# Performance work log

Hardware: AMD Instinct MI355X
Metric: run time of the kernel (lower is better)

## Reference

```python
import jax, jax.numpy as jnp
import numpy as np

P = 22536   # priors
B = 32      # batch
M = 16      # objects per image (fixed for jit)
C = 81      # classes incl. background
THRESHOLD = 0.5
ALPHA_REG = 1.0   # config.reg_weights
FL_ALPHA = 0.25
FL_GAMMA = 2.0
EPS = 1e-7


def cxcy_to_xy(c):
    return jnp.concatenate([c[..., :2] - c[..., 2:] / 2, c[..., :2] + c[..., 2:] / 2], -1)


def gcxgcy_to_cxcy(g, p):
    return jnp.concatenate([g[..., :2] * p[..., 2:] / 10 + p[..., :2],
                            jnp.exp(g[..., 2:] / 5) * p[..., 2:]], -1)


def iou_xy(a, b):
    # a: (M,4) xyxy, b: (P,4) xyxy -> (M,P)
    lt = jnp.maximum(a[:, None, :2], b[None, :, :2])
    rb = jnp.minimum(a[:, None, 2:], b[None, :, 2:])
    inter = jnp.prod(jnp.clip(rb - lt, 0.0), -1)
    area_a = jnp.prod(a[:, 2:] - a[:, :2], -1)
    area_b = jnp.prod(b[:, 2:] - b[:, :2], -1)
    return inter / (area_a[:, None] + area_b[None, :] - inter)


def diou_loss(p, g):
    # elementwise DIoU loss, p/g: (..., 4) xyxy -> (...)
    lt = jnp.maximum(p[..., :2], g[..., :2])
    rb = jnp.minimum(p[..., 2:], g[..., 2:])
    inter = jnp.prod(jnp.clip(rb - lt, 0.0), -1)
    ap = jnp.prod(p[..., 2:] - p[..., :2], -1)
    ag = jnp.prod(g[..., 2:] - g[..., :2], -1)
    iou = inter / (ap + ag - inter + EPS)
    cp = (p[..., :2] + p[..., 2:]) / 2
    cg = (g[..., :2] + g[..., 2:]) / 2
    d2 = jnp.sum((cp - cg) ** 2, -1)
    elt = jnp.minimum(p[..., :2], g[..., :2])
    erb = jnp.maximum(p[..., 2:], g[..., 2:])
    c2 = jnp.sum((erb - elt) ** 2, -1) + EPS
    return 1.0 - iou + d2 / c2


def match_image(boxes_i, labels_i, priors_xy):
    # boxes_i: (M,4), labels_i: (M,), priors_xy: (P,4)
    overlap = iou_xy(boxes_i, priors_xy)                 # (M,P)
    ofp = overlap.max(0)                                  # overlap_for_each_prior (P,)
    obj = jnp.argmax(overlap, 0)                          # object_for_each_prior (P,)
    pfo = jnp.argmax(overlap, 1)                          # prior_for_each_object (M,)
    obj = obj.at[pfo].set(jnp.arange(M))
    ofp = ofp.at[pfo].set(1.0)
    lab = labels_i[obj]                                   # (P,)
    lab_neg = jnp.where(ofp < THRESHOLD - 0.1, -1, lab)
    lab = jnp.where(ofp < THRESHOLD, 0, lab)
    true_locs = boxes_i[obj]                              # (P,4)
    return lab, lab_neg, true_locs


def setup_inputs() -> dict:
    key = jax.random.key(0)
    k1, k2, k3, k4, k5, k6, k7 = jax.random.split(key, 7)
    pcxy = jax.random.uniform(k1, (P, 2), minval=0.05, maxval=0.95)
    pwh = jax.random.uniform(k2, (P, 2), minval=0.02, maxval=0.3)
    priors_cxcy = jnp.concatenate([pcxy, pwh], -1)
    ctr = jax.random.uniform(k3, (B, M, 2), minval=0.2, maxval=0.8)
    wh = jax.random.uniform(k4, (B, M, 2), minval=0.05, maxval=0.3)
    boxes = jnp.concatenate([ctr - wh / 2, ctr + wh / 2], -1)
    labels = jax.random.randint(k5, (B, M), 1, C).astype(jnp.int32)
    predicted_locs = jax.random.normal(k6, (B, P, 4), dtype=jnp.float32)
    predicted_scores = jax.random.normal(k7, (B, P, C), dtype=jnp.float32)
    return {"predicted_locs": predicted_locs, "predicted_scores": predicted_scores,
            "boxes": boxes, "labels": labels, "priors_cxcy": priors_cxcy}


def reference(predicted_locs, predicted_scores, boxes, labels, priors_cxcy):
    priors_xy = cxcy_to_xy(priors_cxcy)
    lab, lab_neg, true_locs = jax.vmap(match_image, in_axes=(0, 0, None))(boxes, labels, priors_xy)
    decoded = cxcy_to_xy(gcxgcy_to_cxcy(predicted_locs, priors_cxcy))   # (B,P,4)
    pos = lab > 0
    neg = lab_neg == -1
    # DIoU localization loss, mean over positive priors
    loc = diou_loss(decoded, true_locs)                                 # (B,P)
    npos = jnp.maximum(pos.sum(), 1)
    loc_loss = jnp.sum(loc * pos) / npos
    # focal classification loss over union of positive and hard-negative priors
    logp = jax.nn.log_softmax(predicted_scores, -1)                     # (B,P,C)
    lp_t = jnp.take_along_axis(logp, lab[..., None], -1)[..., 0]        # (B,P)
    pt = jnp.exp(lp_t)
    fl = FL_ALPHA * (1.0 - pt) ** FL_GAMMA * (-lp_t)
    m = pos | neg
    conf_loss = jnp.sum(fl * m) / jnp.maximum(m.sum(), 1)
    return conf_loss + ALPHA_REG * loc_loss
```

## Files before the change

kernel.cpp:

```cpp
#include <hip/hip_runtime.h>
#include <math.h>

#define PN 22536
#define BN 32
#define MN 16
#define CN 81
#define NMB ((PN + 255) / 256)
#define NCB 2048

#if __has_builtin(__builtin_amdgcn_exp2f)
#define EXP2(x) __builtin_amdgcn_exp2f(x)
#else
#define EXP2(x) exp2f(x)
#endif
#if __has_builtin(__builtin_amdgcn_logf)
#define LOG2(x) __builtin_amdgcn_logf(x)
#else
#define LOG2(x) log2f(x)
#endif

__global__ __launch_bounds__(256)
void pfo_kernel(const float* __restrict__ boxes,
                const float* __restrict__ priors,
                unsigned long long* __restrict__ pfo_key)
{
    const int b = blockIdx.y;
    const int p = blockIdx.x * 256 + threadIdx.x;

    __shared__ float4 sbox[MN];
    __shared__ float  sarea[MN];
    __shared__ unsigned long long skey[MN];
    if (threadIdx.x < MN) {
        float4 bx = reinterpret_cast<const float4*>(boxes)[b * MN + threadIdx.x];
        sbox[threadIdx.x]  = bx;
        sarea[threadIdx.x] = (bx.z - bx.x) * (bx.w - bx.y);
        skey[threadIdx.x]  = 0ull;
    }
    __syncthreads();

    float x0 = 0.f, y0 = 0.f, x1 = 0.f, y1 = 0.f, ab = 0.f;
    const bool valid = (p < PN);
    if (valid) {
        float4 pc = reinterpret_cast<const float4*>(priors)[p];
        float hw = pc.z / 2.0f, hh = pc.w / 2.0f;
        x0 = pc.x - hw; y0 = pc.y - hh;
        x1 = pc.x + hw; y1 = pc.y + hh;
        ab = (x1 - x0) * (y1 - y0);
    }

    const int lane = threadIdx.x & 63;
    #pragma unroll
    for (int m = 0; m < MN; ++m) {
        unsigned long long key = 0ull;
        if (valid) {
            float4 bx = sbox[m];
            float lx = fmaxf(bx.x, x0), ly = fmaxf(bx.y, y0);
            float rx = fminf(bx.z, x1), ry = fminf(bx.w, y1);
            float inter = fmaxf(rx - lx, 0.0f) * fmaxf(ry - ly, 0.0f);
            float iou = inter / (sarea[m] + ab - inter);
            key = ((unsigned long long)__float_as_uint(iou) << 32) |
                  (unsigned long long)(~(unsigned int)p);
        }
        #pragma unroll
        for (int off = 32; off >= 1; off >>= 1) {
            unsigned long long o = __shfl_down(key, (unsigned)off, 64);
            if (o > key) key = o;
        }
        if (lane == 0) atomicMax(&skey[m], key);
    }
    __syncthreads();
    if (threadIdx.x < MN)
        atomicMax(&pfo_key[b * MN + threadIdx.x], skey[threadIdx.x]);
}

__global__ __launch_bounds__(256)
void match_kernel(const float* __restrict__ boxes,
                  const int*   __restrict__ labels,
                  const float* __restrict__ priors,
                  const float* __restrict__ plocs,
                  const unsigned long long* __restrict__ pfo_key,
                  unsigned char* __restrict__ labbyte,
                  float4* __restrict__ mpart)
{
    const int b = blockIdx.y;
    const int p = blockIdx.x * 256 + threadIdx.x;

    __shared__ float4 sbox[MN];
    __shared__ float  sarea[MN];
    __shared__ int    slab[MN];
    __shared__ int    spfo[MN];
    __shared__ float  sred[4][3];

    if (threadIdx.x < MN) {
        float4 bx = reinterpret_cast<const float4*>(boxes)[b * MN + threadIdx.x];
        sbox[threadIdx.x]  = bx;
        sarea[threadIdx.x] = (bx.z - bx.x) * (bx.w - bx.y);
        slab[threadIdx.x]  = labels[b * MN + threadIdx.x];
        spfo[threadIdx.x]  = (int)(~(unsigned int)(pfo_key[b * MN + threadIdx.x] &
                                                   0xFFFFFFFFull));
    }
    __syncthreads();

    float loc = 0.f, mc = 0.f, psc = 0.f;
    if (p < PN) {
        float4 pc = reinterpret_cast<const float4*>(priors)[p];
        float hw = pc.z / 2.0f, hh = pc.w / 2.0f;
        float qx0 = pc.x - hw, qy0 = pc.y - hh;
        float qx1 = pc.x + hw, qy1 = pc.y + hh;
        float ab  = (qx1 - qx0) * (qy1 - qy0);

        float best = -1.0f;
        int bestm = 0;
        #pragma unroll
        for (int m = 0; m < MN; ++m) {
            float4 bx = sbox[m];
            float lx = fmaxf(bx.x, qx0), ly = fmaxf(bx.y, qy0);
            float rx = fminf(bx.z, qx1), ry = fminf(bx.w, qy1);
            float inter = fmaxf(rx - lx, 0.0f) * fmaxf(ry - ly, 0.0f);
            float iou = inter / (sarea[m] + ab - inter);
            if (iou > best) { best = iou; bestm = m; }
        }
        #pragma unroll
        for (int m = 0; m < MN; ++m)
            if (spfo[m] == p) { bestm = m; best = 1.0f; }

        bool pos = best >= 0.5f;
        bool neg = best < 0.4f;
        labbyte[(size_t)b * PN + p] =
            pos ? (unsigned char)slab[bestm] : (neg ? (unsigned char)0
                                                    : (unsigned char)255);
        if (pos || neg) mc = 1.0f;

        if (pos) {
            float4 g = reinterpret_cast<const float4*>(plocs)[(size_t)b * PN + p];
            float cx = g.x * pc.z / 10.0f + pc.x;
            float cy = g.y * pc.w / 10.0f + pc.y;
            float ww = expf(g.z / 5.0f) * pc.z;
            float hh2 = expf(g.w / 5.0f) * pc.w;
            float px0 = cx - ww / 2.0f, py0 = cy - hh2 / 2.0f;
            float px1 = cx + ww / 2.0f, py1 = cy + hh2 / 2.0f;

            float4 gb = sbox[bestm];
            float lx = fmaxf(px0, gb.x), ly = fmaxf(py0, gb.y);
            float rx = fminf(px1, gb.z), ry = fminf(py1, gb.w);
            float inter = fmaxf(rx - lx, 0.f) * fmaxf(ry - ly, 0.f);
            float apx = (px1 - px0) * (py1 - py0);
            float agx = (gb.z - gb.x) * (gb.w - gb.y);
            float iou = inter / (apx + agx - inter + 1e-7f);
            float cpx = (px0 + px1) / 2.0f, cpy = (py0 + py1) / 2.0f;
            float cgx = (gb.x + gb.z) / 2.0f, cgy = (gb.y + gb.w) / 2.0f;
            float dx = cpx - cgx, dy = cpy - cgy;
            float d2 = dx * dx + dy * dy;
            float ex0 = fminf(px0, gb.x), ey0 = fminf(py0, gb.y);
            float ex1 = fmaxf(px1, gb.z), ey1 = fmaxf(py1, gb.w);
            float ew = ex1 - ex0, eh = ey1 - ey0;
            float c2 = ew * ew + eh * eh + 1e-7f;
            loc = 1.0f - iou + d2 / c2;
            psc = 1.0f;
        }
    }

    #pragma unroll
    for (int off = 32; off >= 1; off >>= 1) {
        loc += __shfl_down(loc, (unsigned)off, 64);
        mc  += __shfl_down(mc,  (unsigned)off, 64);
        psc += __shfl_down(psc, (unsigned)off, 64);
    }
    const int lane = threadIdx.x & 63;
    const int w = threadIdx.x >> 6;
    if (lane == 0) { sred[w][0] = loc; sred[w][1] = mc; sred[w][2] = psc; }
    __syncthreads();
    if (threadIdx.x == 0) {
        float a = 0.f, bsum = 0.f, c = 0.f;
        #pragma unroll
        for (int i = 0; i < 4; ++i) {
            a += sred[i][0]; bsum += sred[i][1]; c += sred[i][2];
        }
        mpart[b * NMB + blockIdx.x] = make_float4(a, c, bsum, 0.f);
    }
}

__global__ __launch_bounds__(256)
void conf_kernel(const float* __restrict__ scores,
                 const unsigned char* __restrict__ labbyte,
                 float* __restrict__ cpart)
{
    const int lane = threadIdx.x & 63;
    const int j    = lane & 15;
    const int g    = (lane >> 4);
    const int wave_g = (blockIdx.x * 256 + threadIdx.x) >> 6;
    const int stride = NCB * 16;
    const int R = BN * PN;

    const float LOG2E = 1.4426950408889634f;
    const float LN2   = 0.6931471805599453f;

    float conf = 0.f;

    for (int base = wave_g * 4; base < R; base += stride) {
        const int row = base + g;
        const unsigned int lb4 =
            *reinterpret_cast<const unsigned int*>(labbyte + base);
        const int lb  = (int)((lb4 >> (8 * g)) & 0xFFu);
        const int lbe = (lb == 255) ? 0 : lb;

        const float* srow = scores + (size_t)row * CN;
        float s0 = srow[j]      * LOG2E;
        float s1 = srow[j + 16] * LOG2E;
        float s2 = srow[j + 32] * LOG2E;
        float s3 = srow[j + 48] * LOG2E;
        float s4 = srow[j + 64] * LOG2E;
        float s5 = (j == 0) ? srow[80] * LOG2E : -INFINITY;

        float mx = fmaxf(fmaxf(fmaxf(s0, s1), fmaxf(s2, s3)), fmaxf(s4, s5));
        #pragma unroll
        for (int off = 1; off < 16; off <<= 1)
            mx = fmaxf(mx, __shfl_xor(mx, off, 64));

        float es = EXP2(s0 - mx) + EXP2(s1 - mx) + EXP2(s2 - mx) +
                   EXP2(s3 - mx) + EXP2(s4 - mx) + EXP2(s5 - mx);
        #pragma unroll
        for (int off = 1; off < 16; off <<= 1)
            es += __shfl_xor(es, off, 64);

        int hi = lbe >> 4, lo = lbe & 15;
        float sel = s0;
        sel = (hi == 1) ? s1 : sel;
        sel = (hi == 2) ? s2 : sel;
        sel = (hi == 3) ? s3 : sel;
        sel = (hi == 4) ? s4 : sel;
        sel = (hi == 5) ? s5 : sel;
        float st = __shfl(sel, (lane & 48) | lo, 64);

        float q  = st - mx - LOG2(es);
        float pt = EXP2(q);
        float lp = q * LN2;
        float om = 1.0f - pt;
        float w  = (lb != 255) ? 1.0f : 0.0f;
        if (j == 0) conf += w * 0.25f * om * om * (-lp);
    }

    #pragma unroll
    for (int off = 1; off < 64; off <<= 1)
        conf += __shfl_xor(conf, off, 64);

    __shared__ float sred[4];
    if (lane == 0) sred[threadIdx.x >> 6] = conf;
    __syncthreads();
    if (threadIdx.x == 0)
        cpart[blockIdx.x] = sred[0] + sred[1] + sred[2] + sred[3];
}

__global__ __launch_bounds__(256)
void reduce_kernel(const float4* __restrict__ mpart,
                   const float*  __restrict__ cpart,
                   float* __restrict__ out)
{
    const int NM = BN * NMB;
    float loc = 0.f, pcnt = 0.f, mcnt = 0.f, conf = 0.f;
    for (int i = threadIdx.x; i < NM; i += 256) {
        float4 v = mpart[i];
        loc += v.x; pcnt += v.y; mcnt += v.z;
    }
    for (int i = threadIdx.x; i < NCB; i += 256)
        conf += cpart[i];

    #pragma unroll
    for (int off = 1; off < 64; off <<= 1) {
        loc  += __shfl_xor(loc,  off, 64);
        pcnt += __shfl_xor(pcnt, off, 64);
        mcnt += __shfl_xor(mcnt, off, 64);
        conf += __shfl_xor(conf, off, 64);
    }
    __shared__ float s[4][4];
    int lane = threadIdx.x & 63, w = threadIdx.x >> 6;
    if (lane == 0) { s[w][0] = loc; s[w][1] = pcnt; s[w][2] = mcnt; s[w][3] = conf; }
    __syncthreads();
    if (threadIdx.x == 0) {
        float L = 0.f, Pc = 0.f, Mc = 0.f, Cf = 0.f;
        #pragma unroll
        for (int i = 0; i < 4; ++i) {
            L += s[i][0]; Pc += s[i][1]; Mc += s[i][2]; Cf += s[i][3];
        }
        out[0] = Cf / fmaxf(Mc, 1.0f) + L / fmaxf(Pc, 1.0f);
    }
}

extern "C" void kernel_launch(void* const* d_in, const int* in_sizes, int n_in,
                              void* d_out, int out_size, void* d_ws, size_t ws_size,
                              hipStream_t stream)
{
    const float* plocs  = (const float*)d_in[0];
    const float* scores = (const float*)d_in[1];
    const float* boxes  = (const float*)d_in[2];
    const int*   labels = (const int*)d_in[3];
    const float* priors = (const float*)d_in[4];
    float* out = (float*)d_out;

    char* ws = (char*)d_ws;
    unsigned long long* pfo_key = (unsigned long long*)ws;
    unsigned char* labbyte = (unsigned char*)(ws + 4096);
    float4* mpart = (float4*)(ws + 4096 + 721152);
    float*  cpart = (float*)(ws + 4096 + 721152 + BN * NMB * 16);

    hipMemsetAsync(pfo_key, 0, BN * MN * sizeof(unsigned long long), stream);

    dim3 gA(NMB, BN);
    pfo_kernel<<<gA, 256, 0, stream>>>(boxes, priors, pfo_key);
    match_kernel<<<gA, 256, 0, stream>>>(boxes, labels, priors, plocs,
                                         pfo_key, labbyte, mpart);
    conf_kernel<<<NCB, 256, 0, stream>>>(scores, labbyte, cpart);
    reduce_kernel<<<1, 256, 0, stream>>>(mpart, cpart, out);
}
```

Baseline: 382.8 us.

## Fuse focal classification loss into match kernel with LDS-staged score rows

The separate conf kernel and the label-byte workspace are removed. Each match block now computes the focal loss for its own 256 priors, staging 8 score rows at a time into shared memory with coalesced float4 loads, and writes the conf partial sum alongside the localization partials. The pfo kernel replaces the 64-bit key shuffle reduction with a float max reduction plus a ballot, so only one lane issues the atomic. This saves a global write and read of labels and a kernel launch, and it improves score-load coalescing. The cost is a longer, heavier match kernel that relies on intra-wave shared-memory ordering with no barrier.

```diff
diff --git a/kernel.cpp b/kernel.cpp
--- a/kernel.cpp
+++ b/kernel.cpp
@@ -6,7 +6,6 @@
 #define MN 16
 #define CN 81
 #define NMB ((PN + 255) / 256)
-#define NCB 2048
 
 #if __has_builtin(__builtin_amdgcn_exp2f)
 #define EXP2(x) __builtin_amdgcn_exp2f(x)
@@ -51,22 +50,26 @@
     const int lane = threadIdx.x & 63;
     #pragma unroll
     for (int m = 0; m < MN; ++m) {
-        unsigned long long key = 0ull;
+        float iou = -INFINITY;
         if (valid) {
             float4 bx = sbox[m];
             float lx = fmaxf(bx.x, x0), ly = fmaxf(bx.y, y0);
             float rx = fminf(bx.z, x1), ry = fminf(bx.w, y1);
             float inter = fmaxf(rx - lx, 0.0f) * fmaxf(ry - ly, 0.0f);
-            float iou = inter / (sarea[m] + ab - inter);
-            key = ((unsigned long long)__float_as_uint(iou) << 32) |
-                  (unsigned long long)(~(unsigned int)p);
-        }
-        #pragma unroll
-        for (int off = 32; off >= 1; off >>= 1) {
-            unsigned long long o = __shfl_down(key, (unsigned)off, 64);
-            if (o > key) key = o;
-        }
-        if (lane == 0) atomicMax(&skey[m], key);
+            iou = inter / (sarea[m] + ab - inter);
+        }
+        float mx = iou;
+        #pragma unroll
+        for (int off = 1; off < 64; off <<= 1)
+            mx = fmaxf(mx, __shfl_xor(mx, off, 64));
+        unsigned long long mask = __ballot(iou == mx);
+        int lane0 = (int)__ffsll((unsigned long long)mask) - 1;
+        if (valid && lane == lane0) {
+            unsigned long long key =
+                ((unsigned long long)__float_as_uint(iou) << 32) |
+                (unsigned long long)(~(unsigned int)p);
+            atomicMax(&skey[m], key);
+        }
     }
     __syncthreads();
     if (threadIdx.x < MN)
@@ -74,22 +77,25 @@
 }
 
 __global__ __launch_bounds__(256)
-void match_kernel(const float* __restrict__ boxes,
-                  const int*   __restrict__ labels,
-                  const float* __restrict__ priors,
-                  const float* __restrict__ plocs,
-                  const unsigned long long* __restrict__ pfo_key,
-                  unsigned char* __restrict__ labbyte,
-                  float4* __restrict__ mpart)
+void match_conf_kernel(const float* __restrict__ boxes,
+                       const int*   __restrict__ labels,
+                       const float* __restrict__ priors,
+                       const float* __restrict__ plocs,
+                       const float* __restrict__ scores,
+                       const unsigned long long* __restrict__ pfo_key,
+                       float4* __restrict__ mpart)
 {
-    const int b = blockIdx.y;
-    const int p = blockIdx.x * 256 + threadIdx.x;
+    const int b  = blockIdx.y;
+    const int p0 = blockIdx.x * 256;
+    const int p  = p0 + threadIdx.x;
 
     __shared__ float4 sbox[MN];
     __shared__ float  sarea[MN];
     __shared__ int    slab[MN];
     __shared__ int    spfo[MN];
-    __shared__ float  sred[4][3];
+    __shared__ unsigned char slb[256];
+    __shared__ float4 spack4[4][162];
+    __shared__ float  sred[4][4];
 
     if (threadIdx.x < MN) {
         float4 bx = reinterpret_cast<const float4*>(boxes)[b * MN + threadIdx.x];
@@ -102,6 +108,7 @@
     __syncthreads();
 
     float loc = 0.f, mc = 0.f, psc = 0.f;
+    unsigned char myl = 255;
     if (p < PN) {
         float4 pc = reinterpret_cast<const float4*>(priors)[p];
         float hw = pc.z / 2.0f, hh = pc.w / 2.0f;
@@ -126,9 +133,8 @@
 
         bool pos = best >= 0.5f;
         bool neg = best < 0.4f;
-        labbyte[(size_t)b * PN + p] =
-            pos ? (unsigned char)slab[bestm] : (neg ? (unsigned char)0
-                                                    : (unsigned char)255);
+        myl = pos ? (unsigned char)slab[bestm]
+                  : (neg ? (unsigned char)0 : (unsigned char)255);
         if (pos || neg) mc = 1.0f;
 
         if (pos) {
@@ -159,6 +165,7 @@
             psc = 1.0f;
         }
     }
+    slb[threadIdx.x] = myl;
 
     #pragma unroll
     for (int off = 32; off >= 1; off >>= 1) {
@@ -167,103 +174,87 @@
         psc += __shfl_down(psc, (unsigned)off, 64);
     }
     const int lane = threadIdx.x & 63;
-    const int w = threadIdx.x >> 6;
+    const int w    = threadIdx.x >> 6;
     if (lane == 0) { sred[w][0] = loc; sred[w][1] = mc; sred[w][2] = psc; }
     __syncthreads();
-    if (threadIdx.x == 0) {
-        float a = 0.f, bsum = 0.f, c = 0.f;
-        #pragma unroll
-        for (int i = 0; i < 4; ++i) {
-            a += sred[i][0]; bsum += sred[i][1]; c += sred[i][2];
-        }
-        mpart[b * NMB + blockIdx.x] = make_float4(a, c, bsum, 0.f);
-    }
-}
-
-__global__ __launch_bounds__(256)
-void conf_kernel(const float* __restrict__ scores,
-                 const unsigned char* __restrict__ labbyte,
-                 float* __restrict__ cpart)
-{
-    const int lane = threadIdx.x & 63;
-    const int j    = lane & 15;
-    const int g    = (lane >> 4);
-    const int wave_g = (blockIdx.x * 256 + threadIdx.x) >> 6;
-    const int stride = NCB * 16;
-    const int R = BN * PN;
-
+
+    const int g8 = lane >> 3;
+    const int j  = lane & 7;
     const float LOG2E = 1.4426950408889634f;
     const float LN2   = 0.6931471805599453f;
 
-    float conf = 0.f;
-
-    for (int base = wave_g * 4; base < R; base += stride) {
-        const int row = base + g;
-        const unsigned int lb4 =
-            *reinterpret_cast<const unsigned int*>(labbyte + base);
-        const int lb  = (int)((lb4 >> (8 * g)) & 0xFFu);
-        const int lbe = (lb == 255) ? 0 : lb;
-
-        const float* srow = scores + (size_t)row * CN;
-        float s0 = srow[j]      * LOG2E;
-        float s1 = srow[j + 16] * LOG2E;
-        float s2 = srow[j + 32] * LOG2E;
-        float s3 = srow[j + 48] * LOG2E;
-        float s4 = srow[j + 64] * LOG2E;
-        float s5 = (j == 0) ? srow[80] * LOG2E : -INFINITY;
-
-        float mx = fmaxf(fmaxf(fmaxf(s0, s1), fmaxf(s2, s3)), fmaxf(s4, s5));
-        #pragma unroll
-        for (int off = 1; off < 16; off <<= 1)
-            mx = fmaxf(mx, __shfl_xor(mx, off, 64));
-
-        float es = EXP2(s0 - mx) + EXP2(s1 - mx) + EXP2(s2 - mx) +
-                   EXP2(s3 - mx) + EXP2(s4 - mx) + EXP2(s5 - mx);
-        #pragma unroll
-        for (int off = 1; off < 16; off <<= 1)
-            es += __shfl_xor(es, off, 64);
-
-        int hi = lbe >> 4, lo = lbe & 15;
-        float sel = s0;
-        sel = (hi == 1) ? s1 : sel;
-        sel = (hi == 2) ? s2 : sel;
-        sel = (hi == 3) ? s3 : sel;
-        sel = (hi == 4) ? s4 : sel;
-        sel = (hi == 5) ? s5 : sel;
-        float st = __shfl(sel, (lane & 48) | lo, 64);
-
-        float q  = st - mx - LOG2(es);
-        float pt = EXP2(q);
-        float lp = q * LN2;
-        float om = 1.0f - pt;
-        float w  = (lb != 255) ? 1.0f : 0.0f;
-        if (j == 0) conf += w * 0.25f * om * om * (-lp);
+    float confs = 0.f;
+    for (int it = 0; it < 8; ++it) {
+        const int prow = w * 64 + it * 8;
+        const int gp   = p0 + prow;
+        if (gp < PN) {
+            const size_t fbase = ((size_t)b * PN + gp) * (size_t)CN;
+            const float4* gsrc = reinterpret_cast<const float4*>(scores + fbase);
+            float4* dst = spack4[w];
+            dst[lane]      = gsrc[lane];
+            dst[lane + 64] = gsrc[lane + 64];
+            if (lane < 34) dst[lane + 128] = gsrc[lane + 128];
+            const float* rowp =
+                reinterpret_cast<const float*>(spack4[w]) + g8 * 81;
+
+            float v[10];
+            #pragma unroll
+            for (int k = 0; k < 10; ++k) v[k] = rowp[j + 8 * k];
+            float v80 = (j == 0) ? rowp[80] : -INFINITY;
+
+            float mx = v80;
+            #pragma unroll
+            for (int k = 0; k < 10; ++k) mx = fmaxf(mx, v[k]);
+            #pragma unroll
+            for (int off = 1; off < 8; off <<= 1)
+                mx = fmaxf(mx, __shfl_xor(mx, off, 64));
+
+            const float mx2 = mx * LOG2E;
+            float es = EXP2(fmaf(v80, LOG2E, -mx2));
+            #pragma unroll
+            for (int k = 0; k < 10; ++k)
+                es += EXP2(fmaf(v[k], LOG2E, -mx2));
+            #pragma unroll
+            for (int off = 1; off < 8; off <<= 1)
+                es += __shfl_xor(es, off, 64);
+
+            const int lb  = slb[prow + g8];
+            const int lbe = (lb == 255) ? 0 : lb;
+            const float st = rowp[lbe];
+            float q  = fmaf(st, LOG2E, -mx2) - LOG2(es);
+            float pt = EXP2(q);
+            float om = 1.0f - pt;
+            float fl = 0.25f * om * om * (-(q * LN2));
+            if (j == 0 && lb != 255) confs += fl;
+        }
     }
 
     #pragma unroll
     for (int off = 1; off < 64; off <<= 1)
-        conf += __shfl_xor(conf, off, 64);
-
-    __shared__ float sred[4];
-    if (lane == 0) sred[threadIdx.x >> 6] = conf;
-    __syncthreads();
-    if (threadIdx.x == 0)
-        cpart[blockIdx.x] = sred[0] + sred[1] + sred[2] + sred[3];
+        confs += __shfl_xor(confs, off, 64);
+    if (lane == 0) sred[w][3] = confs;
+    __syncthreads();
+
+    if (threadIdx.x == 0) {
+        float a = 0.f, bsum = 0.f, c = 0.f, cf = 0.f;
+        #pragma unroll
+        for (int i = 0; i < 4; ++i) {
+            a += sred[i][0]; bsum += sred[i][1]; c += sred[i][2]; cf += sred[i][3];
+        }
+        mpart[b * NMB + blockIdx.x] = make_float4(a, c, bsum, cf);
+    }
 }
 
 __global__ __launch_bounds__(256)
 void reduce_kernel(const float4* __restrict__ mpart,
-                   const float*  __restrict__ cpart,
                    float* __restrict__ out)
 {
     const int NM = BN * NMB;
     float loc = 0.f, pcnt = 0.f, mcnt = 0.f, conf = 0.f;
     for (int i = threadIdx.x; i < NM; i += 256) {
         float4 v = mpart[i];
-        loc += v.x; pcnt += v.y; mcnt += v.z;
-    }
-    for (int i = threadIdx.x; i < NCB; i += 256)
-        conf += cpart[i];
+        loc += v.x; pcnt += v.y; mcnt += v.z; conf += v.w;
+    }
 
     #pragma unroll
     for (int off = 1; off < 64; off <<= 1) {
@@ -299,16 +290,13 @@
 
     char* ws = (char*)d_ws;
     unsigned long long* pfo_key = (unsigned long long*)ws;
-    unsigned char* labbyte = (unsigned char*)(ws + 4096);
-    float4* mpart = (float4*)(ws + 4096 + 721152);
-    float*  cpart = (float*)(ws + 4096 + 721152 + BN * NMB * 16);
+    float4* mpart = (float4*)(ws + 4096);
 
     hipMemsetAsync(pfo_key, 0, BN * MN * sizeof(unsigned long long), stream);
 
     dim3 gA(NMB, BN);
     pfo_kernel<<<gA, 256, 0, stream>>>(boxes, priors, pfo_key);
-    match_kernel<<<gA, 256, 0, stream>>>(boxes, labels, priors, plocs,
-                                         pfo_key, labbyte, mpart);
-    conf_kernel<<<NCB, 256, 0, stream>>>(scores, labbyte, cpart);
-    reduce_kernel<<<1, 256, 0, stream>>>(mpart, cpart, out);
+    match_conf_kernel<<<gA, 256, 0, stream>>>(boxes, labels, priors, plocs,
+                                              scores, pfo_key, mpart);
+    reduce_kernel<<<1, 256, 0, stream>>>(mpart, out);
 }
```

Result: faster. 358.9 us, median of 2 (-6.2%).
